# Optimization experiments

Measured on AMD Instinct MI355X. Metric: run time of the kernel, lower is better.

The kernel has to match this reference:

```python
import jax, jax.numpy as jnp
import numpy as np

ALPHA = 0.3          # triplet margin
LOSS_WEIGHT = 1.0
VALID_COST = 100.0   # chosen so all queries are valid (query2gt ~ U[0,1))
POS_T = 3            # pos_thresh
NEG_T = 30           # neg_thresh
EPS = 1e-6           # torch pairwise_distance eps


def setup_inputs() -> dict:
    key0 = jax.random.key(0)
    ks = jax.random.split(key0, 6)
    Nq, V, K, D, G = 2048, 6, 4096, 256, 64
    attn = jax.random.normal(ks[0], (Nq, V, K), dtype=jnp.float32)
    query2gt = jax.random.uniform(ks[1], (Nq, G), dtype=jnp.float32)  # min < VALID_COST always
    query = jax.random.normal(ks[2], (Nq, V, D), dtype=jnp.float32)
    key = jax.random.normal(ks[3], (K, V, D), dtype=jnp.float32)
    pos_idx = jax.random.randint(ks[4], (V * Nq,), 0, POS_T, dtype=jnp.int64 if jax.config.jax_enable_x64 else jnp.int32)
    neg_idx = jax.random.randint(ks[5], (V * Nq,), POS_T, NEG_T, dtype=jnp.int64 if jax.config.jax_enable_x64 else jnp.int32)
    return {"attn": attn, "query2gt": query2gt, "query": query, "key": key,
            "pos_idx": pos_idx, "neg_idx": neg_idx}


def reference(attn, query2gt, query, key, pos_idx, neg_idx):
    # valid filtering: query2gt.min(-1) < VALID_COST is all-True by construction,
    # so no rows are dropped (keeps shapes static under jit).
    q = jnp.transpose(query, (1, 0, 2))   # [V, Nq, D]
    k = jnp.transpose(key, (1, 0, 2))     # [V, K, D]
    a = jnp.transpose(attn, (1, 0, 2))    # [V, Nq, K]
    V, Nq, K = a.shape

    # batched euclidean cdist per view via gram expansion
    qq = jnp.sum(q * q, axis=-1)[:, :, None]          # [V, Nq, 1]
    kk = jnp.sum(k * k, axis=-1)[:, None, :]          # [V, 1, K]
    d2 = qq + kk - 2.0 * jnp.einsum('vnd,vkd->vnk', q, k)
    dist = jnp.sqrt(jnp.maximum(d2, 0.0))             # [V, Nq, K]

    sorted_idx = jnp.argsort(dist, axis=-1).reshape(V * Nq, K)
    a = a.reshape(V * Nq, K)
    r = jnp.arange(V * Nq)

    pos = jax.nn.sigmoid(a[r, sorted_idx[r, pos_idx]])  # [V*Nq]
    neg = jax.nn.sigmoid(a[r, sorted_idx[r, neg_idx]])  # [V*Nq]

    # TripletMarginLoss(margin=ALPHA, p=1) with anchor = ones, 1-d embeddings
    d_pos = jnp.abs(1.0 - pos + EPS)
    d_neg = jnp.abs(1.0 - neg + EPS)
    loss = jnp.mean(jnp.maximum(d_pos - d_neg + ALPHA, 0.0))
    return LOSS_WEIGHT * loss
```

## Files before the change

kernel.cpp:

```cpp
#include <hip/hip_runtime.h>
#include <stdint.h>

#define NQ    2048
#define VV    6
#define KCNT  4096
#define DD    256
#define NROWS (VV*NQ)
#define ALPHA_M 0.3f
#define EPSL  1e-6f
#define SBIAS 256.0f
#define ZTHR  2.05f
#define CAP   256

#define TM 128
#define TN 128
#define BKK 32

typedef _Float16 f16x8 __attribute__((ext_vector_type(8)));
typedef _Float16 f16x4 __attribute__((ext_vector_type(4)));
typedef float    f32x4 __attribute__((ext_vector_type(4)));

__device__ __forceinline__ void gload16(const void* g, void* l) {
    __builtin_amdgcn_global_load_lds(
        (__attribute__((address_space(1))) void*)(uintptr_t)g,
        (__attribute__((address_space(3))) void*)(uintptr_t)(uint32_t)(uintptr_t)l,
        16, 0, 0);
}

__device__ __forceinline__ unsigned ord16(_Float16 h) {
    unsigned short b = __builtin_bit_cast(unsigned short, h);
    return (b & 0x8000u) ? (unsigned)(~b & 0xFFFFu) : (unsigned)(b | 0x8000u);
}

__device__ __forceinline__ float triplet_term(const float* attn, int r, int kpos, int kneg) {
    int v = r / NQ, q = r - v * NQ;
    float apos = attn[(size_t)q * (VV*KCNT) + v*KCNT + kpos];
    float aneg = attn[(size_t)q * (VV*KCNT) + v*KCNT + kneg];
    float pv = 1.0f / (1.0f + expf(-apos));
    float nv = 1.0f / (1.0f + expf(-aneg));
    float dp = fabsf(1.0f - pv + EPSL);
    float dn = fabsf(1.0f - nv + EPSL);
    return fmaxf(dp - dn + ALPHA_M, 0.0f);
}

__global__ __launch_bounds__(256) void pack_fused(const float* __restrict__ key,
                                                  const float* __restrict__ query,
                                                  _Float16* __restrict__ Bpack,
                                                  _Float16* __restrict__ Apack,
                                                  float* __restrict__ kkp,
                                                  float* __restrict__ Trow,
                                                  unsigned* __restrict__ fcount,
                                                  float* __restrict__ out)
{
    int wid  = threadIdx.x >> 6;
    int lane = threadIdx.x & 63;
    if (blockIdx.x < 6144) {
        int rowid = blockIdx.x * 4 + wid;
        int k = rowid / 6;
        int v = rowid - k * 6;
        float4 x = *(const float4*)(key + (size_t)rowid * DD + lane * 4);
        f16x4 h;
        h.x = (_Float16)x.x; h.y = (_Float16)x.y;
        h.z = (_Float16)x.z; h.w = (_Float16)x.w;
        *(f16x4*)(Bpack + ((size_t)(v * KCNT + k)) * DD + lane * 4) = h;

        float s = x.x*x.x + x.y*x.y + x.z*x.z + x.w*x.w;
        #pragma unroll
        for (int off = 32; off >= 1; off >>= 1) s += __shfl_xor(s, off);
        if (lane == 0) kkp[v * KCNT + k] = s;
    } else {
        int bid2 = blockIdx.x - 6144;
        if (bid2 == 0) {
            if (threadIdx.x == 0) *fcount = 0;
            if (threadIdx.x == 1) out[0] = 0.0f;
        }
        int rowid = bid2 * 4 + wid;
        int q = rowid / 6;
        int v = rowid - q * 6;
        float4 x = *(const float4*)(query + (size_t)rowid * DD + lane * 4);
        f16x4 h;
        h.x = (_Float16)x.x; h.y = (_Float16)x.y;
        h.z = (_Float16)x.z; h.w = (_Float16)x.w;
        *(f16x4*)(Apack + ((size_t)(v * NQ + q)) * DD + lane * 4) = h;

        float qq = x.x*x.x + x.y*x.y + x.z*x.z + x.w*x.w;
        #pragma unroll
        for (int off = 32; off >= 1; off >>= 1) qq += __shfl_xor(qq, off);
        if (lane == 0)
            Trow[v * NQ + q] = 256.0f - ZTHR * sqrtf(512.0f + 4.0f * qq);
    }
}

__global__ __launch_bounds__(256) void score_gemm(const _Float16* __restrict__ Apack,
                                                  const _Float16* __restrict__ Bpack,
                                                  const float* __restrict__ kkp,
                                                  const float* __restrict__ Trow,
                                                  unsigned long long* __restrict__ maskbT,
                                                  _Float16* __restrict__ wsf)
{
    __shared__ _Float16 As[TM * BKK];
    __shared__ _Float16 Bs[TN * BKK];
    __shared__ unsigned long long lmask[TM][2];

    int tid  = threadIdx.x;
    int wid  = tid >> 6;
    int lane = tid & 63;

    int fid = blockIdx.y * 32 + blockIdx.x;
    int swz = (fid & 7) * 384 + (fid >> 3);
    int bx  = swz & 31;
    int by  = swz >> 5;

    int c0   = bx * TN;
    int grow = by * TM;
    int v    = grow / NQ;
    int q0   = grow - v * NQ;

    int srow = (wid << 4) + (lane >> 2);
    int sseg = (lane & 3) ^ ((lane >> 2) & 3);
    const _Float16* Ag0 = Apack + ((size_t)(v*NQ   + q0 + srow)) * DD + sseg*8;
    const _Float16* Ag1 = Ag0 + (size_t)64 * DD;
    const _Float16* Bg0 = Bpack + ((size_t)(v*KCNT + c0 + srow)) * DD + sseg*8;
    const _Float16* Bg1 = Bg0 + (size_t)64 * DD;

    _Float16* lA0 = As + wid*512;
    _Float16* lA1 = As + 2048 + wid*512;
    _Float16* lB0 = Bs + wid*512;
    _Float16* lB1 = Bs + 2048 + wid*512;

    int fr = lane & 15;
    int kg = lane >> 4;
    int rb = (wid >> 1) * 64;
    int cb = (wid & 1) * 64;
    int rg = lane >> 4;
    int ksw = (kg ^ (fr & 3)) << 3;

    f32x4 acc[4][4] = {};

    for (int kb = 0; kb < DD; kb += BKK) {
        __syncthreads();
        gload16(Ag0 + kb, lA0);
        gload16(Ag1 + kb, lA1);
        gload16(Bg0 + kb, lB0);
        gload16(Bg1 + kb, lB1);
        __syncthreads();

        f16x8 af[4], bf[4];
        #pragma unroll
        for (int m = 0; m < 4; ++m)
            af[m] = *(const f16x8*)&As[(rb + m*16 + fr)*BKK + ksw];
        #pragma unroll
        for (int n = 0; n < 4; ++n)
            bf[n] = *(const f16x8*)&Bs[(cb + n*16 + fr)*BKK + ksw];
        #pragma unroll
        for (int m = 0; m < 4; ++m)
            #pragma unroll
            for (int n = 0; n < 4; ++n)
                acc[m][n] = __builtin_amdgcn_mfma_f32_16x16x32_f16(af[m], bf[n], acc[m][n], 0, 0, 0);
    }

    int cl = wid & 1;
    float kkv[4];
    #pragma unroll
    for (int n = 0; n < 4; ++n)
        kkv[n] = kkp[v*KCNT + c0 + cb + n*16 + fr];

    int sh = rg * 16;

    #pragma unroll
    for (int m = 0; m < 4; ++m) {
        #pragma unroll
        for (int j = 0; j < 4; ++j) {
            int lr = rb + m*16 + rg*4 + j;
            int gr = grow + lr;
            float Tr = Trow[gr];
            unsigned long long mk = 0;
            #pragma unroll
            for (int n = 0; n < 4; ++n) {
                float s = kkv[n] - 2.0f * acc[m][n][j];
                wsf[(size_t)gr * KCNT + (c0 + cb + n*16 + fr)] = (_Float16)(s - SBIAS);
                unsigned long long bal = __ballot(s < Tr);
                mk |= (unsigned long long)((unsigned)(bal >> sh) & 0xFFFFu) << (n*16);
            }
            if (fr == 0) lmask[lr][cl] = mk;
        }
    }
    __syncthreads();

    if (tid < TM)
        maskbT[(size_t)(bx*2 + 0) * NROWS + grow + tid]         = lmask[tid][0];
    else
        maskbT[(size_t)(bx*2 + 1) * NROWS + grow + (tid - TM)]  = lmask[tid - TM][1];
}

__global__ __launch_bounds__(256) void select2_kernel(const unsigned long long* __restrict__ maskbT,
                                                      const _Float16* __restrict__ wsf,
                                                      const float* __restrict__ attn,
                                                      const int* __restrict__ pos_idx,
                                                      const int* __restrict__ neg_idx,
                                                      unsigned* __restrict__ fcount,
                                                      int* __restrict__ flist,
                                                      float* __restrict__ out)
{
    __shared__ unsigned cbuf[4][CAP];
    __shared__ float bsum;
    if (threadIdx.x == 0) bsum = 0.0f;
    __syncthreads();

    int wid  = threadIdx.x >> 6;
    int lane = threadIdx.x & 63;
    int r    = blockIdx.x * 4 + wid;
    int p = pos_idx[r];
    int n = neg_idx[r];

    unsigned long long mk = maskbT[(size_t)lane * NROWS + r];
    unsigned c_l = (unsigned)__popcll(mk);
    unsigned pre = c_l;
    #pragma unroll
    for (int off = 1; off <= 32; off <<= 1) {
        unsigned o = __shfl_up(pre, off);
        if (lane >= off) pre += o;
    }
    unsigned total = __shfl(pre, 63);
    unsigned excl  = pre - c_l;

    if (total < (unsigned)(n + 1) || total > CAP) {
        if (lane == 0) {
            unsigned i = atomicAdd(fcount, 1u);
            flist[i] = r;
        }
    } else {
        unsigned* mybuf = cbuf[wid];
        const _Float16* srow = wsf + (size_t)r * KCNT + (lane << 6);
        unsigned idx = excl;
        unsigned long long t = mk;
        while (t) {
            int b = __ffsll((long long)t) - 1;
            t &= t - 1;
            _Float16 h = srow[b];
            mybuf[idx++] = (ord16(h) << 12) | (unsigned)((lane << 6) + b);
        }
        __asm__ volatile("s_waitcnt lgkmcnt(0)" ::: "memory");

        unsigned v0 = (lane       < (int)total) ? mybuf[lane]       : 0xFFFFFFFFu;
        unsigned v1 = (lane + 64  < (int)total) ? mybuf[lane + 64]  : 0xFFFFFFFFu;
        unsigned v2 = (lane + 128 < (int)total) ? mybuf[lane + 128] : 0xFFFFFFFFu;
        unsigned v3 = (lane + 192 < (int)total) ? mybuf[lane + 192] : 0xFFFFFFFFu;
        int kpos = 0, kneg = 0;
        for (int t2 = 0; t2 <= n; ++t2) {
            unsigned m01 = v0 < v1 ? v0 : v1;
            unsigned m23 = v2 < v3 ? v2 : v3;
            unsigned m = m01 < m23 ? m01 : m23;
            #pragma unroll
            for (int off = 32; off >= 1; off >>= 1) {
                unsigned o = __shfl_xor(m, off);
                m = o < m ? o : m;
            }
            if      (v0 == m) v0 = 0xFFFFFFFFu;
            else if (v1 == m) v1 = 0xFFFFFFFFu;
            else if (v2 == m) v2 = 0xFFFFFFFFu;
            else if (v3 == m) v3 = 0xFFFFFFFFu;
            if (t2 == p) kpos = (int)(m & 0xFFFu);
            if (t2 == n) kneg = (int)(m & 0xFFFu);
        }
        if (lane == 0)
            atomicAdd(&bsum, triplet_term(attn, r, kpos, kneg) * (1.0f / (float)NROWS));
    }
    __syncthreads();
    if (threadIdx.x == 0) atomicAdd(out, bsum);
}

__global__ __launch_bounds__(256) void fallback_kernel(const _Float16* __restrict__ Apack,
                                                       const _Float16* __restrict__ Bpack,
                                                       const float* __restrict__ kkp,
                                                       const float* __restrict__ attn,
                                                       const int* __restrict__ pos_idx,
                                                       const int* __restrict__ neg_idx,
                                                       const unsigned* __restrict__ fcount,
                                                       const int* __restrict__ flist,
                                                       float* __restrict__ out)
{
    __shared__ float qrow[DD];
    __shared__ unsigned keys[KCNT];
    int nf = (int)*fcount;
    for (int it = blockIdx.x; it < nf; it += gridDim.x) {
        int r = flist[it];
        int v = r / NQ, q = r - v * NQ;
        qrow[threadIdx.x] = (float)Apack[((size_t)(v*NQ + q)) * DD + threadIdx.x];
        __syncthreads();
        for (int i = 0; i < 16; ++i) {
            int c = i * 256 + threadIdx.x;
            float dot = 0.0f;
            const f16x8* bp = (const f16x8*)(Bpack + ((size_t)(v*KCNT + c)) * DD);
            for (int d8 = 0; d8 < 32; ++d8) {
                f16x8 b = bp[d8];
                #pragma unroll
                for (int j = 0; j < 8; ++j) dot += qrow[d8*8 + j] * (float)b[j];
            }
            float s = kkp[v*KCNT + c] - 2.0f * dot;
            keys[c] = (ord16((_Float16)(s - SBIAS)) << 12) | (unsigned)c;
        }
        __syncthreads();
        if (threadIdx.x < 64) {
            int lane = threadIdx.x;
            int p = pos_idx[r], n = neg_idx[r];
            unsigned prev = 0;
            int kpos = 0, kneg = 0;
            for (int t = 0; t <= n; ++t) {
                unsigned m = 0xFFFFFFFFu;
                for (int i = 0; i < 64; ++i) {
                    unsigned kk2 = keys[i*64 + lane];
                    if (kk2 > prev && kk2 < m) m = kk2;
                }
                #pragma unroll
                for (int off = 32; off >= 1; off >>= 1) {
                    unsigned o = __shfl_xor(m, off);
                    m = o < m ? o : m;
                }
                if (t == p) kpos = (int)(m & 0xFFFu);
                if (t == n) kneg = (int)(m & 0xFFFu);
                prev = m;
            }
            if (lane == 0)
                atomicAdd(out, triplet_term(attn, r, kpos, kneg) * (1.0f / (float)NROWS));
        }
        __syncthreads();
    }
}

extern "C" void kernel_launch(void* const* d_in, const int* in_sizes, int n_in,
                              void* d_out, int out_size, void* d_ws, size_t ws_size,
                              hipStream_t stream)
{
    const float* attn    = (const float*)d_in[0];
    const float* query   = (const float*)d_in[2];
    const float* key     = (const float*)d_in[3];
    const int*   pos_idx = (const int*)d_in[4];
    const int*   neg_idx = (const int*)d_in[5];
    float* out = (float*)d_out;

    char* w = (char*)d_ws;
    unsigned*           fcount = (unsigned*)(w);
    float*              Trow   = (float*)   (w + 256);
    float*              kkp    = (float*)   (w + 49408);
    int*                flist  = (int*)     (w + 147712);
    unsigned long long* maskbT = (unsigned long long*)(w + 196864);
    _Float16*           Apack  = (_Float16*)(w + 6488320);
    _Float16*           Bpack  = (_Float16*)(w + 12779776);
    _Float16*           wsf    = (_Float16*)(w + 25362688);

    pack_fused<<<9216, 256, 0, stream>>>(key, query, Bpack, Apack, kkp, Trow,
                                         fcount, out);

    dim3 gg(KCNT / TN, NROWS / TM);
    score_gemm<<<gg, 256, 0, stream>>>(Apack, Bpack, kkp, Trow, maskbT, wsf);

    select2_kernel<<<NROWS / 4, 256, 0, stream>>>(maskbT, wsf, attn, pos_idx, neg_idx,
                                                  fcount, flist, out);
    fallback_kernel<<<16, 256, 0, stream>>>(Apack, Bpack, kkp, attn, pos_idx, neg_idx,
                                            fcount, flist, out);
}
```

Baseline: 125.5 us.

## Load MFMA operands directly from global memory, bypassing LDS staging

Removes the shared-memory staging of A and B tiles and their per-iteration barriers in the score GEMM. Each wave now reads its f16x8 fragments straight from global memory through per-row pointers, with the K loop fully unrolled. This drops LDS traffic and synchronization but loses cross-wave reuse: each A and B row is now fetched by two waves, so the kernel depends on L1/L2 hits to absorb the extra global loads.

```diff
diff --git a/kernel.cpp b/kernel.cpp
--- a/kernel.cpp
+++ b/kernel.cpp
@@ -14,18 +14,10 @@
 
 #define TM 128
 #define TN 128
-#define BKK 32
 
 typedef _Float16 f16x8 __attribute__((ext_vector_type(8)));
 typedef _Float16 f16x4 __attribute__((ext_vector_type(4)));
 typedef float    f32x4 __attribute__((ext_vector_type(4)));
-
-__device__ __forceinline__ void gload16(const void* g, void* l) {
-    __builtin_amdgcn_global_load_lds(
-        (__attribute__((address_space(1))) void*)(uintptr_t)g,
-        (__attribute__((address_space(3))) void*)(uintptr_t)(uint32_t)(uintptr_t)l,
-        16, 0, 0);
-}
 
 __device__ __forceinline__ unsigned ord16(_Float16 h) {
     unsigned short b = __builtin_bit_cast(unsigned short, h);
@@ -98,8 +90,6 @@
                                                   unsigned long long* __restrict__ maskbT,
                                                   _Float16* __restrict__ wsf)
 {
-    __shared__ _Float16 As[TM * BKK];
-    __shared__ _Float16 Bs[TN * BKK];
     __shared__ unsigned long long lmask[TM][2];
 
     int tid  = threadIdx.x;
@@ -115,43 +105,31 @@
     int grow = by * TM;
     int v    = grow / NQ;
     int q0   = grow - v * NQ;
-
-    int srow = (wid << 4) + (lane >> 2);
-    int sseg = (lane & 3) ^ ((lane >> 2) & 3);
-    const _Float16* Ag0 = Apack + ((size_t)(v*NQ   + q0 + srow)) * DD + sseg*8;
-    const _Float16* Ag1 = Ag0 + (size_t)64 * DD;
-    const _Float16* Bg0 = Bpack + ((size_t)(v*KCNT + c0 + srow)) * DD + sseg*8;
-    const _Float16* Bg1 = Bg0 + (size_t)64 * DD;
-
-    _Float16* lA0 = As + wid*512;
-    _Float16* lA1 = As + 2048 + wid*512;
-    _Float16* lB0 = Bs + wid*512;
-    _Float16* lB1 = Bs + 2048 + wid*512;
 
     int fr = lane & 15;
     int kg = lane >> 4;
     int rb = (wid >> 1) * 64;
     int cb = (wid & 1) * 64;
     int rg = lane >> 4;
-    int ksw = (kg ^ (fr & 3)) << 3;
+
+    const f16x8* Ap[4];
+    const f16x8* Bp[4];
+    #pragma unroll
+    for (int m = 0; m < 4; ++m)
+        Ap[m] = (const f16x8*)(Apack + ((size_t)(v*NQ + q0 + rb + m*16 + fr)) * DD + kg*8);
+    #pragma unroll
+    for (int n = 0; n < 4; ++n)
+        Bp[n] = (const f16x8*)(Bpack + ((size_t)(v*KCNT + c0 + cb + n*16 + fr)) * DD + kg*8);
 
     f32x4 acc[4][4] = {};
 
-    for (int kb = 0; kb < DD; kb += BKK) {
-        __syncthreads();
-        gload16(Ag0 + kb, lA0);
-        gload16(Ag1 + kb, lA1);
-        gload16(Bg0 + kb, lB0);
-        gload16(Bg1 + kb, lB1);
-        __syncthreads();
-
+    #pragma unroll
+    for (int t = 0; t < 8; ++t) {
         f16x8 af[4], bf[4];
         #pragma unroll
-        for (int m = 0; m < 4; ++m)
-            af[m] = *(const f16x8*)&As[(rb + m*16 + fr)*BKK + ksw];
-        #pragma unroll
-        for (int n = 0; n < 4; ++n)
-            bf[n] = *(const f16x8*)&Bs[(cb + n*16 + fr)*BKK + ksw];
+        for (int m = 0; m < 4; ++m) af[m] = Ap[m][t*4];
+        #pragma unroll
+        for (int n = 0; n < 4; ++n) bf[n] = Bp[n][t*4];
         #pragma unroll
         for (int m = 0; m < 4; ++m)
             #pragma unroll
```

Result: slower. 176.1 us (+40.2%).
